# Kernel optimization log

Hardware: AMD Instinct MI355X
Metric: run time of the kernel (lower is better)

Reference implementation:

```python
import jax, jax.numpy as jnp
import numpy as np

N_NODES = 100000
N_EDGES = 1600000
IN_DIM = 165
HIDDEN = 128
OUT_DIM = 2


def gcn_conv(x, W, b, src, dst, n_nodes):
    """PyG GCNConv: h = x @ W; add self-loops; sym-normalized scatter-add; + bias."""
    h = x @ W  # [N, F_out]
    loop = jnp.arange(n_nodes, dtype=src.dtype)
    src_f = jnp.concatenate([src, loop])  # [E + N]
    dst_f = jnp.concatenate([dst, loop])
    deg = jax.ops.segment_sum(jnp.ones(src_f.shape[0], dtype=h.dtype), dst_f,
                              num_segments=n_nodes)  # in-degree incl. self-loop
    dinv = jnp.where(deg > 0, jax.lax.rsqrt(deg), jnp.zeros_like(deg))
    norm = dinv[src_f] * dinv[dst_f]  # [E + N]
    msg = h[src_f] * norm[:, None]  # gather + scale, [E+N, F_out]
    out = jax.ops.segment_sum(msg, dst_f, num_segments=n_nodes)  # scatter-add
    return out + b


def setup_inputs() -> dict:
    key = jax.random.key(0)
    k_x, k_e, k_w1, k_b1, k_w2, k_b2 = jax.random.split(key, 6)
    x = jax.random.normal(k_x, (N_NODES, IN_DIM), dtype=jnp.float32)
    edge_index = jax.random.randint(k_e, (2, N_EDGES), 0, N_NODES, dtype=jnp.int64)
    # Glorot-like init for linear weights, zeros for bias (PyG defaults)
    W1 = jax.random.normal(k_w1, (IN_DIM, HIDDEN), dtype=jnp.float32) / np.sqrt(IN_DIM)
    b1 = jnp.zeros((HIDDEN,), dtype=jnp.float32)
    W2 = jax.random.normal(k_w2, (HIDDEN, OUT_DIM), dtype=jnp.float32) / np.sqrt(HIDDEN)
    b2 = jnp.zeros((OUT_DIM,), dtype=jnp.float32)
    return {"x": x, "edge_index": edge_index, "W1": W1, "b1": b1, "W2": W2, "b2": b2}


def reference(x, edge_index, W1, b1, W2, b2):
    src, dst = edge_index[0], edge_index[1]
    h = gcn_conv(x, W1, b1, src, dst, N_NODES)
    h = jax.nn.relu(h)
    # dropout: eval mode (training=False) -> identity
    out = gcn_conv(h, W2, b2, src, dst, N_NODES)
    return out
```

## Files before the change

kernel.cpp:

```cpp
#include <hip/hip_runtime.h>
#include <hip/hip_fp16.h>

#define N_NODES 100000
#define N_EDGES 1600000
#define IN_DIM  165
#define HIDDEN  128
#define OUT_DIM 2

#define NBKT 196
#define CHUNK 4096
#define NCHUNK ((N_EDGES + CHUNK - 1) / CHUNK)
#define PADCAP 10240
#define KPAD 176
#define GROWS 64

typedef _Float16 half8_t __attribute__((ext_vector_type(8)));
typedef _Float16 half4_t __attribute__((ext_vector_type(4)));
typedef float floatx4 __attribute__((ext_vector_type(4)));


__global__ __launch_bounds__(512) void k_part2(const int* __restrict__ src,
                                               const int* __restrict__ dst,
                                               int* __restrict__ bcnt,
                                               unsigned* __restrict__ arena) {
    __shared__ int hist[256];
    __shared__ int gbase[256];

    int t = threadIdx.x;
    int e0 = blockIdx.x * CHUNK;
    int nE = N_EDGES - e0; if (nE > CHUNK) nE = CHUNK;
    int n4 = nE >> 2;
    const int4* dst4 = (const int4*)(dst + e0);
    const int4* src4 = (const int4*)(src + e0);

    if (t < 256) hist[t] = 0;
    __syncthreads();

    for (int i = t; i < n4; i += 512) {
        int4 d = dst4[i];
        atomicAdd(&hist[d.x >> 9], 1);
        atomicAdd(&hist[d.y >> 9], 1);
        atomicAdd(&hist[d.z >> 9], 1);
        atomicAdd(&hist[d.w >> 9], 1);
    }
    __syncthreads();

    if (t < NBKT) gbase[t] = t * PADCAP + atomicAdd(&bcnt[t], hist[t]);
    if (t < 256) hist[t] = 0;
    __syncthreads();

    for (int i = t; i < n4; i += 512) {
        int4 d = dst4[i];
        int4 s = src4[i];
        #pragma unroll
        for (int j = 0; j < 4; j++) {
            int dd = (j == 0) ? d.x : (j == 1) ? d.y : (j == 2) ? d.z : d.w;
            int ss = (j == 0) ? s.x : (j == 1) ? s.y : (j == 2) ? s.z : s.w;
            int bk = dd >> 9;
            unsigned entry = (unsigned)ss | ((unsigned)(dd & 511) << 17);
            int idx = atomicAdd(&hist[bk], 1);
            arena[gbase[bk] + idx] = entry;
        }
    }
}


__global__ __launch_bounds__(1024) void k_sort4(const unsigned* __restrict__ arena,
                                                const int* __restrict__ bcnt,
                                                int* __restrict__ csr,
                                                int* __restrict__ rowstart,
                                                int* __restrict__ rowend,
                                                float* __restrict__ dinv) {
    __shared__ int cnt[512];
    __shared__ int cur[512];
    __shared__ int wsum[4];
    int b = blockIdx.x;
    int n0 = b << 9;
    int t = threadIdx.x;
    int lane = t & 63, wid = t >> 6;
    int total = bcnt[b];
    int abase = b * PADCAP;
    int dbase = b * PADCAP;
    int nt4 = total >> 2;
    const uint4* arena4 = (const uint4*)(arena + abase);

    if (t < 512) cnt[t] = 0;
    __syncthreads();
    for (int p = t; p < nt4; p += 1024) {
        uint4 e = arena4[p];
        atomicAdd(&cnt[e.x >> 17], 1);
        atomicAdd(&cnt[e.y >> 17], 1);
        atomicAdd(&cnt[e.z >> 17], 1);
        atomicAdd(&cnt[e.w >> 17], 1);
    }
    {
        int p = (nt4 << 2) + t;
        if (p < total) atomicAdd(&cnt[arena[abase + p] >> 17], 1);
    }
    __syncthreads();

    int c0 = 0, c1 = 0, s = 0, inc = 0;
    if (t < 256) {
        c0 = cnt[2 * t];
        c1 = cnt[2 * t + 1];
        s = c0 + c1;
        inc = s;
        #pragma unroll
        for (int off = 1; off < 64; off <<= 1) {
            int y = __shfl_up(inc, off);
            if (lane >= off) inc += y;
        }
        if (lane == 63) wsum[wid] = inc;
    }
    __syncthreads();
    if (t == 0) {
        int acc = 0;
        #pragma unroll
        for (int w = 0; w < 4; w++) { int tv = wsum[w]; wsum[w] = acc; acc += tv; }
    }
    __syncthreads();
    if (t < 256) {
        int base = dbase + wsum[wid] + (inc - s);
        cur[2 * t] = base;
        cur[2 * t + 1] = base + c0;
        int node0 = n0 + 2 * t;
        if (node0 < N_NODES) {
            rowstart[node0] = base;
            rowend[node0] = base + c0;
            dinv[node0] = rsqrtf((float)(c0 + 1));
        }
        if (node0 + 1 < N_NODES) {
            rowstart[node0 + 1] = base + c0;
            rowend[node0 + 1] = base + c0 + c1;
            dinv[node0 + 1] = rsqrtf((float)(c1 + 1));
        }
    }
    __syncthreads();

    for (int p = t; p < nt4; p += 1024) {
        uint4 e = arena4[p];
        #pragma unroll
        for (int j = 0; j < 4; j++) {
            unsigned entry = (j == 0) ? e.x : (j == 1) ? e.y : (j == 2) ? e.z : e.w;
            int local = (int)(entry >> 17);
            int sv = (int)(entry & 0x1FFFFu);
            int pos = atomicAdd(&cur[local], 1);
            csr[pos] = sv;
        }
    }
    {
        int p = (nt4 << 2) + t;
        if (p < total) {
            unsigned entry = arena[abase + p];
            int local = (int)(entry >> 17);
            int sv = (int)(entry & 0x1FFFFu);
            int pos = atomicAdd(&cur[local], 1);
            csr[pos] = sv;
        }
    }
}


__global__ void k_w1t(const float* __restrict__ W1, _Float16* __restrict__ w1t) {
    int idx = blockIdx.x * 256 + threadIdx.x;
    if (idx < HIDDEN * KPAD) {
        int c = idx / KPAD, k = idx - c * KPAD;
        float v = (k < IN_DIM) ? W1[k * HIDDEN + c] : 0.f;
        w1t[idx] = (_Float16)v;
    }
}


__global__ __launch_bounds__(256) void k_gemm1(const float* __restrict__ x,
                                               const _Float16* __restrict__ w1t,
                                               const float* __restrict__ dinv,
                                               _Float16* __restrict__ h1s) {
    __shared__ float xs[GROWS * IN_DIM];
    int t = threadIdx.x;
    int wid = t >> 6, lane = t & 63;
    int row0 = blockIdx.x * GROWS;
    int nrows = N_NODES - row0; if (nrows > GROWS) nrows = GROWS;
    int nflt = nrows * IN_DIM;

    const float4* xb4 = (const float4*)(x + (size_t)row0 * IN_DIM);
    float4* xs4 = (float4*)xs;
    int n4 = nflt >> 2;
    for (int i = t; i < n4; i += 256) xs4[i] = xb4[i];
    for (int i = (n4 << 2) + t; i < nflt; i += 256) xs[i] = x[(size_t)row0 * IN_DIM + i];
    __syncthreads();

    int mrow = wid * 16;
    if (mrow >= nrows) return;
    int m = lane & 15;
    int quad = lane >> 4;
    const float* xrow = xs + (mrow + m) * IN_DIM;
    int grow = row0 + mrow;

    floatx4 acc[8];
    #pragma unroll
    for (int i = 0; i < 8; i++) acc[i] = (floatx4)(0.f);

    #pragma unroll
    for (int kc = 0; kc < 5; kc++) {
        int kb = kc * 32 + quad * 8;
        half8_t a;
        #pragma unroll
        for (int j = 0; j < 8; j++) a[j] = (_Float16)xrow[kb + j];
        #pragma unroll
        for (int cb = 0; cb < 8; cb++) {
            int col = cb * 16 + m;
            half8_t bf = *(const half8_t*)&w1t[col * KPAD + kb];
            acc[cb] = __builtin_amdgcn_mfma_f32_16x16x32_f16(a, bf, acc[cb], 0, 0, 0);
        }
    }
    {
        int kb = 160 + quad * 4;
        half4_t a;
        #pragma unroll
        for (int j = 0; j < 4; j++)
            a[j] = (kb + j < IN_DIM) ? (_Float16)xrow[kb + j] : (_Float16)0.f;
        #pragma unroll
        for (int cb = 0; cb < 8; cb++) {
            int col = cb * 16 + m;
            half4_t bf = *(const half4_t*)&w1t[col * KPAD + kb];
            acc[cb] = __builtin_amdgcn_mfma_f32_16x16x16f16(a, bf, acc[cb], 0, 0, 0);
        }
    }
    float dv[4];
    #pragma unroll
    for (int r = 0; r < 4; r++) dv[r] = dinv[grow + quad * 4 + r];
    #pragma unroll
    for (int cb = 0; cb < 8; cb++) {
        #pragma unroll
        for (int r = 0; r < 4; r++) {
            h1s[(size_t)(grow + quad * 4 + r) * HIDDEN + cb * 16 + m] =
                (_Float16)(acc[cb][r] * dv[r]);
        }
    }
}


__global__ __launch_bounds__(256) void k_agg1(const _Float16* __restrict__ h1,
                                              const int* __restrict__ rowstart,
                                              const int* __restrict__ rowend,
                                              const int* __restrict__ csr,
                                              const float* __restrict__ dinv,
                                              const float* __restrict__ b1,
                                              const float* __restrict__ W2,
                                              float2* __restrict__ h2s) {
    int wid = threadIdx.x >> 6, lane = threadIdx.x & 63;
    int el = lane & 15;
    int es = lane >> 4;
    int node = blockIdx.x * 4 + wid;

    float acc[8];
    {
        half8_t v = *(const half8_t*)(h1 + (size_t)node * HIDDEN + el * 8);
        #pragma unroll
        for (int j = 0; j < 8; j++) acc[j] = (es == 0) ? (float)v[j] : 0.f;
    }

    int p0 = rowstart[node], p1 = rowend[node];
    int p = p0 + es;
    for (; p + 4 < p1; p += 8) {
        int sA = csr[p];
        int sB = csr[p + 4];
        half8_t vA = *(const half8_t*)(h1 + (size_t)sA * HIDDEN + el * 8);
        half8_t vB = *(const half8_t*)(h1 + (size_t)sB * HIDDEN + el * 8);
        #pragma unroll
        for (int j = 0; j < 8; j++) acc[j] += (float)vA[j];
        #pragma unroll
        for (int j = 0; j < 8; j++) acc[j] += (float)vB[j];
    }
    if (p < p1) {
        int s = csr[p];
        half8_t v = *(const half8_t*)(h1 + (size_t)s * HIDDEN + el * 8);
        #pragma unroll
        for (int j = 0; j < 8; j++) acc[j] += (float)v[j];
    }

    #pragma unroll
    for (int j = 0; j < 8; j++) {
        acc[j] += __shfl_xor(acc[j], 16);
        acc[j] += __shfl_xor(acc[j], 32);
    }

    float di = dinv[node];
    float4 bb0 = ((const float4*)b1)[el * 2];
    float4 bb1 = ((const float4*)b1)[el * 2 + 1];
    float bv[8] = {bb0.x, bb0.y, bb0.z, bb0.w, bb1.x, bb1.y, bb1.z, bb1.w};
    float a0 = 0.f, a1 = 0.f;
    #pragma unroll
    for (int j = 0; j < 8; j++) {
        float z = fmaf(di, acc[j], bv[j]);
        float r = fmaxf(z, 0.f);
        float2 w = ((const float2*)W2)[el * 8 + j];
        a0 = fmaf(r, w.x, a0);
        a1 = fmaf(r, w.y, a1);
    }
    #pragma unroll
    for (int off = 8; off; off >>= 1) {
        a0 += __shfl_xor(a0, off);
        a1 += __shfl_xor(a1, off);
    }
    if (lane == 0) h2s[node] = make_float2(di * a0, di * a1);
}


__global__ __launch_bounds__(256) void k_agg2(const float2* __restrict__ h2s,
                                              const int* __restrict__ rowstart,
                                              const int* __restrict__ rowend,
                                              const int* __restrict__ csr,
                                              const float* __restrict__ dinv,
                                              const float* __restrict__ b2,
                                              float2* __restrict__ out) {
    int wid = threadIdx.x >> 6, lane = threadIdx.x & 63;
    int sub = lane >> 4, el = lane & 15;
    int node = blockIdx.x * 16 + wid * 4 + sub;
    int p0 = rowstart[node], p1 = rowend[node];
    float ax = 0.f, ay = 0.f;
    for (int p = p0 + el; p < p1; p += 16) {
        float2 g = h2s[csr[p]];
        ax += g.x;
        ay += g.y;
    }
    #pragma unroll
    for (int off = 8; off; off >>= 1) {
        ax += __shfl_xor(ax, off);
        ay += __shfl_xor(ay, off);
    }
    if (el == 0) {
        float2 self = h2s[node];
        float di = dinv[node];
        out[node] = make_float2(fmaf(di, self.x + ax, b2[0]),
                                fmaf(di, self.y + ay, b2[1]));
    }
}


extern "C" void kernel_launch(void* const* d_in, const int* in_sizes, int n_in,
                              void* d_out, int out_size, void* d_ws, size_t ws_size,
                              hipStream_t stream) {
    const float* x  = (const float*)d_in[0];
    const int*   ei = (const int*)d_in[1];
    const float* W1 = (const float*)d_in[2];
    const float* b1 = (const float*)d_in[3];
    const float* W2 = (const float*)d_in[4];
    const float* b2 = (const float*)d_in[5];
    float* out = (float*)d_out;

    const int* src = ei;
    const int* dst = ei + N_EDGES;

    char* ws = (char*)d_ws;
    size_t off = 0;
    auto alloc = [&](size_t bytes) -> void* {
        void* p = ws + off;
        off += (bytes + 255) & ~(size_t)255;
        return p;
    };
    _Float16* h1s      = (_Float16*)alloc((size_t)N_NODES * HIDDEN * 2);
    float*    dinv     = (float*)   alloc((size_t)N_NODES * 4);
    int*      rowstart = (int*)     alloc((size_t)N_NODES * 4);
    int*      rowend   = (int*)     alloc((size_t)N_NODES * 4);
    int*      bcnt     = (int*)     alloc((size_t)NBKT * 4);
    unsigned* arena    = (unsigned*)alloc((size_t)NBKT * PADCAP * 4);
    int*      csr      = (int*)     alloc((size_t)NBKT * PADCAP * 4);
    _Float16* w1t      = (_Float16*)alloc((size_t)HIDDEN * KPAD * 2);
    float2*   h2s      = (float2*)  alloc((size_t)N_NODES * 8);

    (void)hipMemsetAsync(bcnt, 0, (size_t)NBKT * 4, stream);
    k_w1t<<<(HIDDEN * KPAD + 255) / 256, 256, 0, stream>>>(W1, w1t);
    k_part2<<<NCHUNK, 512, 0, stream>>>(src, dst, bcnt, arena);
    k_sort4<<<NBKT, 1024, 0, stream>>>(arena, bcnt, csr, rowstart, rowend, dinv);
    k_gemm1<<<(N_NODES + GROWS - 1) / GROWS, 256, 0, stream>>>(x, w1t, dinv, h1s);
    k_agg1<<<N_NODES / 4, 256, 0, stream>>>(h1s, rowstart, rowend, csr, dinv, b1, W2, h2s);
    k_agg2<<<N_NODES / 16, 256, 0, stream>>>(h2s, rowstart, rowend, csr, dinv, b2, (float2*)out);
}
```

Measured before the change: 242.6 us.

## Fuse all GCN stages into one persistent cooperative kernel with grid syncs

Wraps the weight transpose, edge partition, bucket sort, GEMM, and both aggregation stages into device functions. It runs them inside a single cooperative persistent kernel separated by grid-wide barriers, replacing the memset and six separate launches. This aims to remove per-launch overhead and inter-kernel gaps. In exchange, each stage runs with 256-thread blocks and a capped grid, so the sort loses parallelism per bucket and occupancy is bound by the shared-memory union. The old multi-kernel path is kept as a fallback.

```diff
diff --git a/kernel.cpp b/kernel.cpp
--- a/kernel.cpp
+++ b/kernel.cpp
@@ -1,5 +1,8 @@
 #include <hip/hip_runtime.h>
 #include <hip/hip_fp16.h>
+#include <hip/hip_cooperative_groups.h>
+
+namespace cg = cooperative_groups;
 
 #define N_NODES 100000
 #define N_EDGES 1600000
@@ -13,21 +16,18 @@
 #define PADCAP 10240
 #define KPAD 176
 #define GROWS 64
+#define NTILE ((N_NODES + GROWS - 1) / GROWS)
 
 typedef _Float16 half8_t __attribute__((ext_vector_type(8)));
 typedef _Float16 half4_t __attribute__((ext_vector_type(4)));
 typedef float floatx4 __attribute__((ext_vector_type(4)));
 
 
-__global__ __launch_bounds__(512) void k_part2(const int* __restrict__ src,
-                                               const int* __restrict__ dst,
-                                               int* __restrict__ bcnt,
-                                               unsigned* __restrict__ arena) {
-    __shared__ int hist[256];
-    __shared__ int gbase[256];
-
-    int t = threadIdx.x;
-    int e0 = blockIdx.x * CHUNK;
+template <int NT>
+__device__ __forceinline__ void part2_chunk(int c, int t, int* hist, int* gbase,
+        const int* __restrict__ src, const int* __restrict__ dst,
+        int* __restrict__ bcnt, unsigned* __restrict__ arena) {
+    int e0 = c * CHUNK;
     int nE = N_EDGES - e0; if (nE > CHUNK) nE = CHUNK;
     int n4 = nE >> 2;
     const int4* dst4 = (const int4*)(dst + e0);
@@ -35,8 +35,7 @@
 
     if (t < 256) hist[t] = 0;
     __syncthreads();
-
-    for (int i = t; i < n4; i += 512) {
+    for (int i = t; i < n4; i += NT) {
         int4 d = dst4[i];
         atomicAdd(&hist[d.x >> 9], 1);
         atomicAdd(&hist[d.y >> 9], 1);
@@ -44,12 +43,10 @@
         atomicAdd(&hist[d.w >> 9], 1);
     }
     __syncthreads();
-
     if (t < NBKT) gbase[t] = t * PADCAP + atomicAdd(&bcnt[t], hist[t]);
     if (t < 256) hist[t] = 0;
     __syncthreads();
-
-    for (int i = t; i < n4; i += 512) {
+    for (int i = t; i < n4; i += NT) {
         int4 d = dst4[i];
         int4 s = src4[i];
         #pragma unroll
@@ -64,19 +61,12 @@
     }
 }
 
-
-__global__ __launch_bounds__(1024) void k_sort4(const unsigned* __restrict__ arena,
-                                                const int* __restrict__ bcnt,
-                                                int* __restrict__ csr,
-                                                int* __restrict__ rowstart,
-                                                int* __restrict__ rowend,
-                                                float* __restrict__ dinv) {
-    __shared__ int cnt[512];
-    __shared__ int cur[512];
-    __shared__ int wsum[4];
-    int b = blockIdx.x;
+template <int NT>
+__device__ __forceinline__ void sort4_bucket(int b, int t, int* cnt, int* cur, int* wsum,
+        const unsigned* __restrict__ arena, const int* __restrict__ bcnt,
+        int* __restrict__ csr, int* __restrict__ rowstart, int* __restrict__ rowend,
+        float* __restrict__ dinv) {
     int n0 = b << 9;
-    int t = threadIdx.x;
     int lane = t & 63, wid = t >> 6;
     int total = bcnt[b];
     int abase = b * PADCAP;
@@ -84,9 +74,9 @@
     int nt4 = total >> 2;
     const uint4* arena4 = (const uint4*)(arena + abase);
 
-    if (t < 512) cnt[t] = 0;
-    __syncthreads();
-    for (int p = t; p < nt4; p += 1024) {
+    for (int i = t; i < 512; i += NT) cnt[i] = 0;
+    __syncthreads();
+    for (int p = t; p < nt4; p += NT) {
         uint4 e = arena4[p];
         atomicAdd(&cnt[e.x >> 17], 1);
         atomicAdd(&cnt[e.y >> 17], 1);
@@ -137,7 +127,7 @@
     }
     __syncthreads();
 
-    for (int p = t; p < nt4; p += 1024) {
+    for (int p = t; p < nt4; p += NT) {
         uint4 e = arena4[p];
         #pragma unroll
         for (int j = 0; j < 4; j++) {
@@ -160,25 +150,11 @@
     }
 }
 
-
-__global__ void k_w1t(const float* __restrict__ W1, _Float16* __restrict__ w1t) {
-    int idx = blockIdx.x * 256 + threadIdx.x;
-    if (idx < HIDDEN * KPAD) {
-        int c = idx / KPAD, k = idx - c * KPAD;
-        float v = (k < IN_DIM) ? W1[k * HIDDEN + c] : 0.f;
-        w1t[idx] = (_Float16)v;
-    }
-}
-
-
-__global__ __launch_bounds__(256) void k_gemm1(const float* __restrict__ x,
-                                               const _Float16* __restrict__ w1t,
-                                               const float* __restrict__ dinv,
-                                               _Float16* __restrict__ h1s) {
-    __shared__ float xs[GROWS * IN_DIM];
-    int t = threadIdx.x;
+__device__ __forceinline__ void gemm1_tile(int tile, int t, float* xs,
+        const float* __restrict__ x, const _Float16* __restrict__ w1t,
+        const float* __restrict__ dinv, _Float16* __restrict__ h1s) {
     int wid = t >> 6, lane = t & 63;
-    int row0 = blockIdx.x * GROWS;
+    int row0 = tile * GROWS;
     int nrows = N_NODES - row0; if (nrows > GROWS) nrows = GROWS;
     int nflt = nrows * IN_DIM;
 
@@ -239,19 +215,13 @@
     }
 }
 
-
-__global__ __launch_bounds__(256) void k_agg1(const _Float16* __restrict__ h1,
-                                              const int* __restrict__ rowstart,
-                                              const int* __restrict__ rowend,
-                                              const int* __restrict__ csr,
-                                              const float* __restrict__ dinv,
-                                              const float* __restrict__ b1,
-                                              const float* __restrict__ W2,
-                                              float2* __restrict__ h2s) {
-    int wid = threadIdx.x >> 6, lane = threadIdx.x & 63;
+__device__ __forceinline__ void agg1_node(int node, int lane,
+        const _Float16* __restrict__ h1, const int* __restrict__ rowstart,
+        const int* __restrict__ rowend, const int* __restrict__ csr,
+        const float* __restrict__ dinv, const float* __restrict__ b1,
+        const float* __restrict__ W2, float2* __restrict__ h2s) {
     int el = lane & 15;
     int es = lane >> 4;
-    int node = blockIdx.x * 4 + wid;
 
     float acc[8];
     {
@@ -306,17 +276,11 @@
     if (lane == 0) h2s[node] = make_float2(di * a0, di * a1);
 }
 
-
-__global__ __launch_bounds__(256) void k_agg2(const float2* __restrict__ h2s,
-                                              const int* __restrict__ rowstart,
-                                              const int* __restrict__ rowend,
-                                              const int* __restrict__ csr,
-                                              const float* __restrict__ dinv,
-                                              const float* __restrict__ b2,
-                                              float2* __restrict__ out) {
-    int wid = threadIdx.x >> 6, lane = threadIdx.x & 63;
-    int sub = lane >> 4, el = lane & 15;
-    int node = blockIdx.x * 16 + wid * 4 + sub;
+__device__ __forceinline__ void agg2_node(int node, int el,
+        const float2* __restrict__ h2s, const int* __restrict__ rowstart,
+        const int* __restrict__ rowend, const int* __restrict__ csr,
+        const float* __restrict__ dinv, const float* __restrict__ b2,
+        float2* __restrict__ out) {
     int p0 = rowstart[node], p1 = rowend[node];
     float ax = 0.f, ay = 0.f;
     for (int p = p0 + el; p < p1; p += 16) {
@@ -335,6 +299,119 @@
         out[node] = make_float2(fmaf(di, self.x + ax, b2[0]),
                                 fmaf(di, self.y + ay, b2[1]));
     }
+}
+
+
+__global__ __launch_bounds__(256, 3) void k_mega(const float* __restrict__ x,
+        const int* __restrict__ src, const int* __restrict__ dst,
+        const float* __restrict__ W1, const float* __restrict__ b1,
+        const float* __restrict__ W2, const float* __restrict__ b2,
+        _Float16* __restrict__ h1s, float* __restrict__ dinv,
+        int* __restrict__ rowstart, int* __restrict__ rowend,
+        int* __restrict__ bcnt, unsigned* __restrict__ arena,
+        int* __restrict__ csr, _Float16* __restrict__ w1t,
+        float2* __restrict__ h2s, float2* __restrict__ outv) {
+    cg::grid_group grid = cg::this_grid();
+    __shared__ union {
+        struct { int hist[256]; int gbase[256]; } p;
+        struct { int cnt[512]; int cur[512]; int wsum[4]; } s;
+        float xs[GROWS * IN_DIM];
+    } sh;
+    int bid = blockIdx.x, t = threadIdx.x, gn = gridDim.x;
+    int lane = t & 63;
+
+    for (int idx = bid * 256 + t; idx < HIDDEN * KPAD; idx += gn * 256) {
+        int c = idx / KPAD, k = idx - c * KPAD;
+        w1t[idx] = (_Float16)((k < IN_DIM) ? W1[k * HIDDEN + c] : 0.f);
+    }
+    if (bid == gn - 1 && t < NBKT) bcnt[t] = 0;
+    grid.sync();
+
+    for (int c = bid; c < NCHUNK; c += gn) {
+        part2_chunk<256>(c, t, sh.p.hist, sh.p.gbase, src, dst, bcnt, arena);
+        __syncthreads();
+    }
+    grid.sync();
+
+    for (int b = bid; b < NBKT; b += gn) {
+        sort4_bucket<256>(b, t, sh.s.cnt, sh.s.cur, sh.s.wsum, arena, bcnt,
+                          csr, rowstart, rowend, dinv);
+        __syncthreads();
+    }
+    grid.sync();
+
+    for (int tile = bid; tile < NTILE; tile += gn) {
+        __syncthreads();
+        gemm1_tile(tile, t, sh.xs, x, w1t, dinv, h1s);
+    }
+    grid.sync();
+
+    for (int nb = bid * 4; nb < N_NODES; nb += gn * 4) {
+        int node = nb + (t >> 6);
+        if (node < N_NODES)
+            agg1_node(node, lane, h1s, rowstart, rowend, csr, dinv, b1, W2, h2s);
+    }
+    grid.sync();
+
+    {
+        int wid = t >> 6, sub = lane >> 4, el = lane & 15;
+        for (int nb = bid * 16; nb < N_NODES; nb += gn * 16) {
+            int node = nb + wid * 4 + sub;
+            if (node < N_NODES)
+                agg2_node(node, el, h2s, rowstart, rowend, csr, dinv, b2, outv);
+        }
+    }
+}
+
+
+__global__ __launch_bounds__(512) void k_part2(const int* __restrict__ src,
+        const int* __restrict__ dst, int* __restrict__ bcnt, unsigned* __restrict__ arena) {
+    __shared__ int hist[256];
+    __shared__ int gbase[256];
+    part2_chunk<512>(blockIdx.x, threadIdx.x, hist, gbase, src, dst, bcnt, arena);
+}
+
+__global__ __launch_bounds__(1024) void k_sort4(const unsigned* __restrict__ arena,
+        const int* __restrict__ bcnt, int* __restrict__ csr, int* __restrict__ rowstart,
+        int* __restrict__ rowend, float* __restrict__ dinv) {
+    __shared__ int cnt[512];
+    __shared__ int cur[512];
+    __shared__ int wsum[4];
+    sort4_bucket<1024>(blockIdx.x, threadIdx.x, cnt, cur, wsum, arena, bcnt,
+                       csr, rowstart, rowend, dinv);
+}
+
+__global__ void k_w1t(const float* __restrict__ W1, _Float16* __restrict__ w1t) {
+    int idx = blockIdx.x * 256 + threadIdx.x;
+    if (idx < HIDDEN * KPAD) {
+        int c = idx / KPAD, k = idx - c * KPAD;
+        w1t[idx] = (_Float16)((k < IN_DIM) ? W1[k * HIDDEN + c] : 0.f);
+    }
+}
+
+__global__ __launch_bounds__(256) void k_gemm1(const float* __restrict__ x,
+        const _Float16* __restrict__ w1t, const float* __restrict__ dinv,
+        _Float16* __restrict__ h1s) {
+    __shared__ float xs[GROWS * IN_DIM];
+    gemm1_tile(blockIdx.x, threadIdx.x, xs, x, w1t, dinv, h1s);
+}
+
+__global__ __launch_bounds__(256) void k_agg1(const _Float16* __restrict__ h1,
+        const int* __restrict__ rowstart, const int* __restrict__ rowend,
+        const int* __restrict__ csr, const float* __restrict__ dinv,
+        const float* __restrict__ b1, const float* __restrict__ W2,
+        float2* __restrict__ h2s) {
+    int node = blockIdx.x * 4 + (threadIdx.x >> 6);
+    agg1_node(node, threadIdx.x & 63, h1, rowstart, rowend, csr, dinv, b1, W2, h2s);
+}
+
+__global__ __launch_bounds__(256) void k_agg2(const float2* __restrict__ h2s,
+        const int* __restrict__ rowstart, const int* __restrict__ rowend,
+        const int* __restrict__ csr, const float* __restrict__ dinv,
+        const float* __restrict__ b2, float2* __restrict__ out) {
+    int wid = threadIdx.x >> 6, lane = threadIdx.x & 63;
+    int node = blockIdx.x * 16 + wid * 4 + (lane >> 4);
+    agg2_node(node, lane & 15, h2s, rowstart, rowend, csr, dinv, b2, out);
 }
 
 
@@ -347,7 +424,7 @@
     const float* b1 = (const float*)d_in[3];
     const float* W2 = (const float*)d_in[4];
     const float* b2 = (const float*)d_in[5];
-    float* out = (float*)d_out;
+    float2* outv = (float2*)d_out;
 
     const int* src = ei;
     const int* dst = ei + N_EDGES;
@@ -369,11 +446,37 @@
     _Float16* w1t      = (_Float16*)alloc((size_t)HIDDEN * KPAD * 2);
     float2*   h2s      = (float2*)  alloc((size_t)N_NODES * 8);
 
-    (void)hipMemsetAsync(bcnt, 0, (size_t)NBKT * 4, stream);
-    k_w1t<<<(HIDDEN * KPAD + 255) / 256, 256, 0, stream>>>(W1, w1t);
-    k_part2<<<NCHUNK, 512, 0, stream>>>(src, dst, bcnt, arena);
-    k_sort4<<<NBKT, 1024, 0, stream>>>(arena, bcnt, csr, rowstart, rowend, dinv);
-    k_gemm1<<<(N_NODES + GROWS - 1) / GROWS, 256, 0, stream>>>(x, w1t, dinv, h1s);
-    k_agg1<<<N_NODES / 4, 256, 0, stream>>>(h1s, rowstart, rowend, csr, dinv, b1, W2, h2s);
-    k_agg2<<<N_NODES / 16, 256, 0, stream>>>(h2s, rowstart, rowend, csr, dinv, b2, (float2*)out);
-}
+    static int coopBlocks = -2;
+    if (coopBlocks == -2) {
+        int nb = 0;
+        if (hipOccupancyMaxActiveBlocksPerMultiprocessor(&nb, k_mega, 256, 0) == hipSuccess
+            && nb > 0)
+            coopBlocks = nb;
+        else
+            coopBlocks = 0;
+    }
+
+    bool launched = false;
+    if (coopBlocks > 0) {
+        int gridn = coopBlocks * 256;
+        if (gridn > 768) gridn = 768;
+        void* kargs[] = {(void*)&x, (void*)&src, (void*)&dst, (void*)&W1, (void*)&b1,
+                         (void*)&W2, (void*)&b2, (void*)&h1s, (void*)&dinv,
+                         (void*)&rowstart, (void*)&rowend, (void*)&bcnt, (void*)&arena,
+                         (void*)&csr, (void*)&w1t, (void*)&h2s, (void*)&outv};
+        hipError_t e = hipLaunchCooperativeKernel((const void*)k_mega, dim3(gridn),
+                                                  dim3(256), kargs, 0, stream);
+        if (e == hipSuccess) launched = true;
+        else coopBlocks = 0;
+    }
+
+    if (!launched) {
+        (void)hipMemsetAsync(bcnt, 0, (size_t)NBKT * 4, stream);
+        k_w1t<<<(HIDDEN * KPAD + 255) / 256, 256, 0, stream>>>(W1, w1t);
+        k_part2<<<NCHUNK, 512, 0, stream>>>(src, dst, bcnt, arena);
+        k_sort4<<<NBKT, 1024, 0, stream>>>(arena, bcnt, csr, rowstart, rowend, dinv);
+        k_gemm1<<<NTILE, 256, 0, stream>>>(x, w1t, dinv, h1s);
+        k_agg1<<<N_NODES / 4, 256, 0, stream>>>(h1s, rowstart, rowend, csr, dinv, b1, W2, h2s);
+        k_agg2<<<N_NODES / 16, 256, 0, stream>>>(h2s, rowstart, rowend, csr, dinv, b2, outv);
+    }
+}
```

New measurement: 631.2 us. +160.2%, slower.
